# Kernel tuning notes

Hardware: AMD Instinct MI355X
Metric: run time of the kernel (lower is better)

Reference implementation:

```python
import jax, jax.numpy as jnp
import numpy as np

N = 100000   # nodes
E = 1600000  # edges
DIN = 100    # input feature dim
D = 64       # hidden dim per GCN layer
G = 512      # graphs in batch
EPS = 1e-5


def setup_inputs() -> dict:
    key = jax.random.key(0)
    ks = jax.random.split(key, 16)
    inp = {}
    inp["x"] = jax.random.normal(ks[0], (N, DIN), dtype=jnp.float32)
    inp["edge_index"] = jax.random.randint(ks[1], (2, E), 0, N)
    inp["edge_weight"] = jax.random.uniform(ks[2], (E,), dtype=jnp.float32)
    inp["batch"] = jnp.sort(jax.random.randint(ks[3], (N,), 0, G))
    dims = [DIN, D, D, D]
    for i in range(3):
        fan_in = dims[i]
        inp[f"w{i}"] = jax.random.normal(ks[4 + i], (dims[i], dims[i + 1]), dtype=jnp.float32) / np.sqrt(fan_in)
        inp[f"b{i}"] = jnp.zeros((dims[i + 1],), dtype=jnp.float32)
        inp[f"g{i}"] = jnp.ones((dims[i + 1],), dtype=jnp.float32)   # BN scale
        inp[f"be{i}"] = jnp.zeros((dims[i + 1],), dtype=jnp.float32)  # BN shift
    inp["out_w"] = jax.random.normal(ks[7], (D, 1), dtype=jnp.float32) / np.sqrt(D)
    inp["out_b"] = jnp.zeros((1,), dtype=jnp.float32)
    return inp


def reference(x, edge_index, edge_weight, batch,
              w0, b0, g0, be0, w1, b1, g1, be1, w2, b2, g2, be2,
              out_w, out_b):
    src, dst = edge_index[0], edge_index[1]
    n = x.shape[0]
    # GCN symmetric normalization with self-loops (PyG gcn_norm, fill_value=1)
    deg = jnp.zeros((n,), dtype=x.dtype).at[dst].add(edge_weight) + 1.0
    dinv = jax.lax.rsqrt(deg)
    norm = edge_weight * dinv[src] * dinv[dst]   # [E]
    self_coeff = dinv * dinv                      # 1/deg, self-loop norm  [N]

    def gcn_bn_relu(h, w, b, g, be):
        h = h @ w + b                                             # linear transform [N,D]
        msg = norm[:, None] * h[src]                              # gather + weight [E,D]
        agg = jnp.zeros_like(h).at[dst].add(msg) + h * self_coeff[:, None]
        mean = agg.mean(axis=0)
        var = agg.var(axis=0)                                     # biased var (torch BN)
        hn = (agg - mean) * jax.lax.rsqrt(var + EPS) * g + be
        return jax.nn.relu(hn)                                    # dropout p=0 -> identity

    h = gcn_bn_relu(x, w0, b0, g0, be0)
    h = gcn_bn_relu(h, w1, b1, g1, be1)
    h = gcn_bn_relu(h, w2, b2, g2, be2)

    # global mean pool per graph
    sums = jax.ops.segment_sum(h, batch, num_segments=G)
    counts = jax.ops.segment_sum(jnp.ones((n, 1), dtype=h.dtype), batch, num_segments=G)
    pooled = sums / jnp.maximum(counts, 1.0)
    return pooled @ out_w + out_b
```

## Files before the change

kernel.cpp:

```cpp
#include <hip/hip_runtime.h>
#include <hip/hip_fp16.h>
#include <cstdint>

#define DH 64
#define EPSV 1e-5f
#define GBLK 2048
#define NBUK 256
#define BROWS 512
#define BINJ 8
#define CAP 12288

__global__ void k_fill(float* __restrict__ p, float v, size_t n) {
  size_t i = blockIdx.x * (size_t)blockDim.x + threadIdx.x;
  if (i < n) p[i] = v;
}

__global__ void k_gcur0(unsigned* __restrict__ gcur0) {
  gcur0[threadIdx.x] = (unsigned)(threadIdx.x * CAP);
}

__global__ __launch_bounds__(256) void k_bin0(
    const int* __restrict__ src, const int* __restrict__ dst,
    const float* __restrict__ ew, unsigned* __restrict__ gcur0,
    unsigned long long* __restrict__ bstage, int E_) {
  __shared__ unsigned cntL[NBUK], offL[NBUK], runL[NBUK];
  const int t = threadIdx.x;
  const int base = blockIdx.x * (256 * BINJ);
  cntL[t] = 0;
  runL[t] = 0;
  __syncthreads();
  unsigned hi[BINJ], lo[BINJ];
  int bb[BINJ];
#pragma unroll
  for (int j = 0; j < BINJ; ++j) {
    int e = base + j * 256 + t;
    bb[j] = -1;
    if (e < E_) {
      int q = dst[e];
      hi[j] = ((unsigned)(q & (BROWS - 1)) << 17) | (unsigned)src[e];
      lo[j] = __float_as_uint(ew[e]);
      bb[j] = q >> 9;
      atomicAdd(&cntL[bb[j]], 1u);
    }
  }
  __syncthreads();
  offL[t] = cntL[t] ? atomicAdd(&gcur0[t], cntL[t]) : 0u;
  __syncthreads();
#pragma unroll
  for (int j = 0; j < BINJ; ++j) {
    if (bb[j] >= 0) {
      unsigned p = offL[bb[j]] + atomicAdd(&runL[bb[j]], 1u);
      bstage[p] = ((unsigned long long)hi[j] << 32) | lo[j];
    }
  }
}

__global__ __launch_bounds__(256) void k_bcnt(
    const unsigned long long* __restrict__ bstage, const unsigned* __restrict__ gcur0,
    int* __restrict__ cnt, float* __restrict__ dinv, float* __restrict__ sc, int N_) {
  __shared__ unsigned cntL[BROWS], degL[BROWS];
  const int b = blockIdx.x, t = threadIdx.x;
  for (int i = t; i < BROWS; i += 256) {
    cntL[i] = 0;
    degL[i] = 0;
  }
  __syncthreads();
  const unsigned beg = (unsigned)(b * CAP), end = gcur0[b];
  for (unsigned p = beg + t; p < end; p += 256) {
    unsigned long long v = bstage[p];
    unsigned r = (unsigned)(v >> 49);
    float w = __uint_as_float((unsigned)v);
    atomicAdd(&cntL[r], 1u);
    atomicAdd(&degL[r], (unsigned)(w * 16777216.0f));
  }
  __syncthreads();
  for (int i = t; i < BROWS; i += 256) {
    int r = b * BROWS + i;
    if (r < N_) {
      float deg = 1.0f + (float)degL[i] * (1.0f / 16777216.0f);
      cnt[r] = (int)cntL[i];
      dinv[r] = rsqrtf(deg);
      sc[r] = 1.0f / deg;
    }
  }
}

__global__ __launch_bounds__(256) void k_scan1(const int* __restrict__ cnt,
                                               int* __restrict__ out,
                                               int* __restrict__ bsums,
                                               int N_, int n1) {
  __shared__ int sm[256];
  const int t = threadIdx.x;
  const int base = blockIdx.x * 1024 + t * 4;
  int v[4], lsum = 0;
#pragma unroll
  for (int j = 0; j < 4; ++j) {
    int i = base + j;
    v[j] = (i < N_) ? ((cnt[i] + 7) & ~7) : 0;
    lsum += v[j];
  }
  sm[t] = lsum;
  __syncthreads();
  for (int o = 1; o < 256; o <<= 1) {
    int x = (t >= o) ? sm[t - o] : 0;
    __syncthreads();
    if (t >= o) sm[t] += x;
    __syncthreads();
  }
  int run = sm[t] - lsum;
#pragma unroll
  for (int j = 0; j < 4; ++j) {
    int i = base + j;
    if (i < n1) out[i] = run;
    run += v[j];
  }
  if (t == 255) bsums[blockIdx.x] = sm[255];
}

__global__ __launch_bounds__(256) void k_scan2(int* __restrict__ bsums, int nb) {
  __shared__ int sm[256];
  int t = threadIdx.x;
  int v = (t < nb) ? bsums[t] : 0;
  sm[t] = v;
  __syncthreads();
  for (int o = 1; o < 256; o <<= 1) {
    int x = (t >= o) ? sm[t - o] : 0;
    __syncthreads();
    if (t >= o) sm[t] += x;
    __syncthreads();
  }
  if (t < nb) bsums[t] = sm[t] - v;
}

__global__ void k_scan3(int* __restrict__ out, const int* __restrict__ bsums, int n1) {
  int i = blockIdx.x * blockDim.x + threadIdx.x;
  if (i < n1) out[i] += bsums[i >> 10];
}

__global__ __launch_bounds__(256) void k_fin(
    const unsigned long long* __restrict__ bstage, const int* __restrict__ rowstart,
    const unsigned* __restrict__ gcur0, const float* __restrict__ dinv,
    unsigned* __restrict__ elist, int N_) {
  __shared__ unsigned lcur[BROWS];
  __shared__ int rsL[BROWS + 1];
  __shared__ float dvL[BROWS];
  const int b = blockIdx.x, t = threadIdx.x;
  const int r0 = b * BROWS;
  for (int i = t; i < BROWS; i += 256) {
    lcur[i] = 0;
    int r = r0 + i;
    dvL[i] = (r < N_) ? dinv[r] : 0.f;
  }
  for (int i = t; i <= BROWS; i += 256) {
    int r = r0 + i;
    if (r > N_) r = N_;
    rsL[i] = rowstart[r];
  }
  __syncthreads();
  const unsigned beg = (unsigned)(b * CAP), end = gcur0[b];
  for (unsigned p = beg + t; p < end; p += 256) {
    unsigned long long v = bstage[p];
    unsigned hi = (unsigned)(v >> 32);
    unsigned r = hi >> 17;
    unsigned s = hi & 0x1FFFFu;
    float w = __uint_as_float((unsigned)v);
    float nm = w * dinv[s] * dvL[r];
    unsigned h15 = (unsigned)__half_as_ushort(__float2half(nm));
    unsigned slot = (unsigned)rsL[r] + atomicAdd(&lcur[r], 1u);
    elist[slot] = (h15 << 17) | s;
  }
  __syncthreads();
  for (int i = t; i < BROWS; i += 256) {
    unsigned p = (unsigned)rsL[i] + lcur[i];
    const unsigned pe = (unsigned)rsL[i + 1];
    for (; p < pe; ++p) elist[p] = 0u;
  }
}

__global__ void k_gbound(const int* __restrict__ batch, int* __restrict__ gstart,
                         int N_, int G_) {
  int i = blockIdx.x * blockDim.x + threadIdx.x;
  if (i >= N_) return;
  int b = batch[i];
  if (i == 0) {
    for (int g = 0; g <= b; ++g) gstart[g] = 0;
  }
  int nb = (i + 1 < N_) ? batch[i + 1] : G_;
  for (int g = b + 1; g <= nb; ++g) gstart[g] = i + 1;
}

template <typename AT>
__global__ __launch_bounds__(256) void k_gemm(
    const AT* __restrict__ A, const float* __restrict__ W,
    const float* __restrict__ bias, const float* __restrict__ stats,
    const float* __restrict__ gam, const float* __restrict__ bet,
    __half* __restrict__ Hh, int n, int K, int fuse, float invN) {
  __shared__ float As[128][17];
  __shared__ float Bs[16][64];
  __shared__ float saL[DH], sbL[DH];
  const int tid = threadIdx.x;
  const int tx = tid & 7;
  const int ty = tid >> 3;
  const int r0 = blockIdx.x * 128;
  if (fuse && tid < DH) {
    float mean = stats[tid] * invN;
    float var = stats[DH + tid] * invN - mean * mean;
    float a = rsqrtf(var + EPSV) * gam[tid];
    saL[tid] = a;
    sbL[tid] = bet[tid] - mean * a;
  }
  if (fuse) __syncthreads();
  float acc[4][8] = {};
  for (int kc = 0; kc < K; kc += 16) {
    for (int idx = tid; idx < 128 * 16; idx += 256) {
      int r = idx >> 4, c = idx & 15;
      int gr = r0 + r, gc = kc + c;
      float v = (gr < n && gc < K) ? (float)A[(size_t)gr * K + gc] : 0.0f;
      if (fuse) v = fmaxf(v * saL[gc] + sbL[gc], 0.0f);
      As[r][c] = v;
    }
    for (int idx = tid; idx < 16 * 64; idx += 256) {
      int r = idx >> 6, c = idx & 63;
      int gr = kc + r;
      Bs[r][c] = (gr < K) ? W[gr * DH + c] : 0.0f;
    }
    __syncthreads();
#pragma unroll
    for (int kk = 0; kk < 16; ++kk) {
      float a[4], b[8];
#pragma unroll
      for (int i = 0; i < 4; ++i) a[i] = As[ty * 4 + i][kk];
#pragma unroll
      for (int j = 0; j < 8; ++j) b[j] = Bs[kk][tx * 8 + j];
#pragma unroll
      for (int i = 0; i < 4; ++i)
#pragma unroll
        for (int j = 0; j < 8; ++j) acc[i][j] += a[i] * b[j];
    }
    __syncthreads();
  }
#pragma unroll
  for (int i = 0; i < 4; ++i) {
    int gr = r0 + ty * 4 + i;
    if (gr < n) {
      float h[8];
#pragma unroll
      for (int j = 0; j < 8; ++j) h[j] = acc[i][j] + bias[tx * 8 + j];
      uint4 o;
      o.x = (unsigned)__half_as_ushort(__float2half(h[0])) |
            ((unsigned)__half_as_ushort(__float2half(h[1])) << 16);
      o.y = (unsigned)__half_as_ushort(__float2half(h[2])) |
            ((unsigned)__half_as_ushort(__float2half(h[3])) << 16);
      o.z = (unsigned)__half_as_ushort(__float2half(h[4])) |
            ((unsigned)__half_as_ushort(__float2half(h[5])) << 16);
      o.w = (unsigned)__half_as_ushort(__float2half(h[6])) |
            ((unsigned)__half_as_ushort(__float2half(h[7])) << 16);
      *reinterpret_cast<uint4*>(&Hh[(size_t)gr * DH + tx * 8]) = o;
    }
  }
}

__global__ __launch_bounds__(256) void k_gather(
    const unsigned* __restrict__ elist, const int* __restrict__ rowstart,
    const __half* __restrict__ Hh, const float* __restrict__ sc,
    __half* __restrict__ AGGh, float* __restrict__ statp, int n) {
  const int wid = threadIdx.x >> 6;
  const int d = threadIdx.x & 63;
  const int gw = blockIdx.x * 4 + wid;
  const int nw = gridDim.x * 4;
  unsigned short* AGGu = (unsigned short*)AGGh;
  float s = 0.f, ss = 0.f;
  for (int row = gw; row < n; row += nw) {
    const int rs = rowstart[row], re = rowstart[row + 1];
    float acc = __half2float(Hh[(size_t)row * DH + d]) * sc[row];
    for (int base = rs; base < re; base += 64) {
      const int rem = re - base;
      unsigned eL = 0u;
      if (d < rem) eL = __builtin_nontemporal_load(&elist[base + d]);
      const int m = rem < 64 ? rem : 64;
      for (int j = 0; j < m; j += 8) {
#pragma unroll
        for (int jj = 0; jj < 8; ++jj) {
          const unsigned e = __shfl(eL, j + jj, 64);
          const float v = __half2float(Hh[(size_t)(e & 0x1FFFFu) * DH + d]);
          const float nm =
              __half2float(__ushort_as_half((unsigned short)(e >> 17)));
          acc = fmaf(nm, v, acc);
        }
      }
    }
    __builtin_nontemporal_store(__half_as_ushort(__float2half(acc)),
                                &AGGu[(size_t)row * DH + d]);
    s += acc;
    ss += acc * acc;
  }
  __shared__ float sm[4][DH], sm2[4][DH];
  sm[wid][d] = s;
  sm2[wid][d] = ss;
  __syncthreads();
  if (threadIdx.x < DH) {
    float a = sm[0][d] + sm[1][d] + sm[2][d] + sm[3][d];
    float b = sm2[0][d] + sm2[1][d] + sm2[2][d] + sm2[3][d];
    __builtin_nontemporal_store(a, &statp[(size_t)blockIdx.x * 128 + d]);
    __builtin_nontemporal_store(b, &statp[(size_t)blockIdx.x * 128 + DH + d]);
  }
}

__global__ __launch_bounds__(256) void k_redstats(const float* __restrict__ statp,
                                                  float* __restrict__ stats, int nblk) {
  const int t = blockIdx.x;
  float s = 0.f;
  for (int b = threadIdx.x; b < nblk; b += 256) s += statp[(size_t)b * 128 + t];
#pragma unroll
  for (int o = 32; o > 0; o >>= 1) s += __shfl_down(s, o, 64);
  __shared__ float sm[4];
  if ((threadIdx.x & 63) == 0) sm[threadIdx.x >> 6] = s;
  __syncthreads();
  if (threadIdx.x == 0) stats[t] = sm[0] + sm[1] + sm[2] + sm[3];
}

__global__ __launch_bounds__(256) void k_poolhead(
    const __half* __restrict__ AGGh, const float* __restrict__ stats,
    const float* __restrict__ gam, const float* __restrict__ bet,
    const float* __restrict__ ow, const int* __restrict__ gstart,
    const float* __restrict__ ob, float* __restrict__ out, float invN) {
  const int g = blockIdx.x;
  const int gs = gstart[g], ge = gstart[g + 1];
  const int wid = threadIdx.x >> 6;
  const int d = threadIdx.x & 63;
  float mean = stats[d] * invN;
  float var = stats[DH + d] * invN - mean * mean;
  float sa = rsqrtf(var + EPSV) * gam[d];
  float sb = bet[d] - mean * sa;
  const float w = ow[d];
  float acc = 0.f;
  for (int row = gs + wid; row < ge; row += 4)
    acc += fmaxf(__half2float(AGGh[(size_t)row * DH + d]) * sa + sb, 0.f) * w;
#pragma unroll
  for (int off = 32; off > 0; off >>= 1) acc += __shfl_down(acc, off, 64);
  __shared__ float sm[4];
  if (d == 0) sm[wid] = acc;
  __syncthreads();
  if (threadIdx.x == 0) {
    float s = sm[0] + sm[1] + sm[2] + sm[3];
    float cnt = (float)(ge - gs);
    out[g] = s / fmaxf(cnt, 1.0f) + ob[0];
  }
}

extern "C" void kernel_launch(void* const* d_in, const int* in_sizes, int n_in,
                              void* d_out, int out_size, void* d_ws, size_t ws_size,
                              hipStream_t stream) {
  const float* x    = (const float*)d_in[0];
  const int*   ei   = (const int*)d_in[1];
  const float* ew   = (const float*)d_in[2];
  const int*   batch= (const int*)d_in[3];
  const float* w0   = (const float*)d_in[4];
  const float* b0   = (const float*)d_in[5];
  const float* g0   = (const float*)d_in[6];
  const float* be0  = (const float*)d_in[7];
  const float* w1   = (const float*)d_in[8];
  const float* b1   = (const float*)d_in[9];
  const float* g1   = (const float*)d_in[10];
  const float* be1  = (const float*)d_in[11];
  const float* w2   = (const float*)d_in[12];
  const float* b2   = (const float*)d_in[13];
  const float* g2   = (const float*)d_in[14];
  const float* be2  = (const float*)d_in[15];
  const float* ow   = (const float*)d_in[16];
  const float* ob   = (const float*)d_in[17];

  const int N_  = in_sizes[3];
  const int E_  = in_sizes[2];
  const int DIN_= in_sizes[0] / N_;
  const int G_  = out_size;
  const int* srcIdx = ei;
  const int* dstIdx = ei + E_;
  const int n1 = N_ + 1;
  const size_t epad = (size_t)E_ + 7ull * N_;

  float* ws = (float*)d_ws;
  size_t off = 0;
  unsigned long long* bstage = (unsigned long long*)(ws + off);
  off += (size_t)2 * NBUK * CAP;
  unsigned* elist = (unsigned*)(ws + off); off += epad;
  float* dinv     = ws + off; off += N_;
  float* sc       = ws + off; off += N_;
  int*   cnt      = (int*)(ws + off); off += N_;
  int*   rowstart = (int*)(ws + off); off += n1 + 1;
  int*   bsums    = (int*)(ws + off); off += 256;
  unsigned* gcur0 = (unsigned*)(ws + off); off += NBUK;
  int*   gstart   = (int*)(ws + off); off += G_ + 1;
  __half* hhalf   = (__half*)(ws + off); off += (size_t)N_ * DH / 2;
  __half* aggh    = (__half*)(ws + off); off += (size_t)N_ * DH / 2;
  float* stats    = ws + off; off += 2 * DH;
  float* statp    = ws + off; off += (size_t)GBLK * 128;
  (void)ws_size; (void)n_in;

  k_gcur0<<<1, NBUK, 0, stream>>>(gcur0);
  k_bin0<<<(E_ + 256 * BINJ - 1) / (256 * BINJ), 256, 0, stream>>>(
      srcIdx, dstIdx, ew, gcur0, bstage, E_);
  k_bcnt<<<NBUK, 256, 0, stream>>>(bstage, gcur0, cnt, dinv, sc, N_);

  const int nb = (n1 + 1023) / 1024;
  k_scan1<<<nb, 256, 0, stream>>>(cnt, rowstart, bsums, N_, n1);
  k_scan2<<<1, 256, 0, stream>>>(bsums, nb);
  k_scan3<<<(n1 + 255) / 256, 256, 0, stream>>>(rowstart, bsums, n1);

  k_fin<<<NBUK, 256, 0, stream>>>(bstage, rowstart, gcur0, dinv, elist, N_);

  k_gbound<<<(N_ + 255) / 256, 256, 0, stream>>>(batch, gstart, N_, G_);

  const float* Wl[3]  = {w0, w1, w2};
  const float* Bl[3]  = {b0, b1, b2};
  const float* Gl[3]  = {g0, g1, g2};
  const float* BeL[3] = {be0, be1, be2};

  const float invN = 1.0f / (float)N_;

  for (int l = 0; l < 3; ++l) {
    if (l == 0) {
      k_gemm<float><<<(N_ + 127) / 128, 256, 0, stream>>>(
          x, Wl[0], Bl[0], stats, nullptr, nullptr, hhalf, N_, DIN_, 0, invN);
    } else {
      k_gemm<__half><<<(N_ + 127) / 128, 256, 0, stream>>>(
          aggh, Wl[l], Bl[l], stats, Gl[l - 1], BeL[l - 1], hhalf, N_, DH, 1, invN);
    }
    k_gather<<<GBLK, 256, 0, stream>>>(elist, rowstart, hhalf, sc, aggh, statp, N_);
    k_redstats<<<128, 256, 0, stream>>>(statp, stats, GBLK);
  }

  k_poolhead<<<G_, 256, 0, stream>>>(aggh, stats, g2, be2, ow, gstart, ob,
                                     (float*)d_out, invN);
}
```

Measured before the change: 385.0 us.

## Replace FP32 SIMT dense transform GEMM with FP16 MFMA kernel

Rewrites the per-layer linear transform to use 16x16x32 f16 MFMA instructions. A and W tiles are staged in LDS as fp16 with an XOR swizzle, K is padded to 128 or 64, and the fused BN+ReLU prologue is kept. The goal is to cut the ALU cost of the dense GEMMs. In exchange it rounds the layer-0 input x and the weights to fp16, and the output is written as scattered 2-byte stores instead of 16-byte vector stores.

```diff
diff --git a/kernel.cpp b/kernel.cpp
--- a/kernel.cpp
+++ b/kernel.cpp
@@ -9,6 +9,9 @@
 #define BROWS 512
 #define BINJ 8
 #define CAP 12288
+
+typedef _Float16 half8 __attribute__((ext_vector_type(8)));
+typedef float f32x4 __attribute__((ext_vector_type(4)));
 
 __global__ void k_fill(float* __restrict__ p, float v, size_t n) {
   size_t i = blockIdx.x * (size_t)blockDim.x + threadIdx.x;
@@ -189,73 +192,103 @@
   for (int g = b + 1; g <= nb; ++g) gstart[g] = i + 1;
 }
 
-template <typename AT>
-__global__ __launch_bounds__(256) void k_gemm(
-    const AT* __restrict__ A, const float* __restrict__ W,
+template <int KP, int FUSE>
+__global__ __launch_bounds__(256) void k_gemm_mfma(
+    const void* __restrict__ Ap, const float* __restrict__ W,
     const float* __restrict__ bias, const float* __restrict__ stats,
     const float* __restrict__ gam, const float* __restrict__ bet,
-    __half* __restrict__ Hh, int n, int K, int fuse, float invN) {
-  __shared__ float As[128][17];
-  __shared__ float Bs[16][64];
+    __half* __restrict__ Hh, int n, int Kreal, float invN) {
+  __shared__ _Float16 Ah[128 * KP];
+  __shared__ _Float16 Bt[64 * KP];
   __shared__ float saL[DH], sbL[DH];
   const int tid = threadIdx.x;
-  const int tx = tid & 7;
-  const int ty = tid >> 3;
   const int r0 = blockIdx.x * 128;
-  if (fuse && tid < DH) {
-    float mean = stats[tid] * invN;
-    float var = stats[DH + tid] * invN - mean * mean;
-    float a = rsqrtf(var + EPSV) * gam[tid];
-    saL[tid] = a;
-    sbL[tid] = bet[tid] - mean * a;
-  }
-  if (fuse) __syncthreads();
-  float acc[4][8] = {};
-  for (int kc = 0; kc < K; kc += 16) {
-    for (int idx = tid; idx < 128 * 16; idx += 256) {
-      int r = idx >> 4, c = idx & 15;
-      int gr = r0 + r, gc = kc + c;
-      float v = (gr < n && gc < K) ? (float)A[(size_t)gr * K + gc] : 0.0f;
-      if (fuse) v = fmaxf(v * saL[gc] + sbL[gc], 0.0f);
-      As[r][c] = v;
-    }
-    for (int idx = tid; idx < 16 * 64; idx += 256) {
-      int r = idx >> 6, c = idx & 63;
-      int gr = kc + r;
-      Bs[r][c] = (gr < K) ? W[gr * DH + c] : 0.0f;
+  if (FUSE) {
+    if (tid < DH) {
+      float mean = stats[tid] * invN;
+      float var = stats[DH + tid] * invN - mean * mean;
+      float a = rsqrtf(var + EPSV) * gam[tid];
+      saL[tid] = a;
+      sbL[tid] = bet[tid] - mean * a;
     }
     __syncthreads();
-#pragma unroll
-    for (int kk = 0; kk < 16; ++kk) {
-      float a[4], b[8];
-#pragma unroll
-      for (int i = 0; i < 4; ++i) a[i] = As[ty * 4 + i][kk];
-#pragma unroll
-      for (int j = 0; j < 8; ++j) b[j] = Bs[kk][tx * 8 + j];
-#pragma unroll
-      for (int i = 0; i < 4; ++i)
-#pragma unroll
-        for (int j = 0; j < 8; ++j) acc[i][j] += a[i] * b[j];
-    }
-    __syncthreads();
-  }
-#pragma unroll
-  for (int i = 0; i < 4; ++i) {
-    int gr = r0 + ty * 4 + i;
-    if (gr < n) {
-      float h[8];
-#pragma unroll
-      for (int j = 0; j < 8; ++j) h[j] = acc[i][j] + bias[tx * 8 + j];
-      uint4 o;
-      o.x = (unsigned)__half_as_ushort(__float2half(h[0])) |
-            ((unsigned)__half_as_ushort(__float2half(h[1])) << 16);
-      o.y = (unsigned)__half_as_ushort(__float2half(h[2])) |
-            ((unsigned)__half_as_ushort(__float2half(h[3])) << 16);
-      o.z = (unsigned)__half_as_ushort(__float2half(h[4])) |
-            ((unsigned)__half_as_ushort(__float2half(h[5])) << 16);
-      o.w = (unsigned)__half_as_ushort(__float2half(h[6])) |
-            ((unsigned)__half_as_ushort(__float2half(h[7])) << 16);
-      *reinterpret_cast<uint4*>(&Hh[(size_t)gr * DH + tx * 8]) = o;
+  }
+  constexpr int KC = KP / 8;
+  for (int ci = tid; ci < 128 * KC; ci += 256) {
+    int row = ci / KC, kc = ci % KC;
+    int gr = r0 + row, k0 = kc * 8;
+    half8 hv;
+    if (FUSE) {
+      const unsigned short* Aa = (const unsigned short*)Ap;
+#pragma unroll
+      for (int j = 0; j < 8; ++j) {
+        int k = k0 + j;
+        float a = (gr < n) ? __half2float(__ushort_as_half(Aa[(size_t)gr * DH + k])) : 0.f;
+        hv[j] = (_Float16)fmaxf(a * saL[k] + sbL[k], 0.f);
+      }
+    } else {
+      const float* Ax = (const float*)Ap;
+#pragma unroll
+      for (int j = 0; j < 8; ++j) {
+        int k = k0 + j;
+        float a = (gr < n && k < Kreal) ? Ax[(size_t)gr * Kreal + k] : 0.f;
+        hv[j] = (_Float16)a;
+      }
+    }
+    *(half8*)&Ah[row * KP + (k0 ^ ((row & 7) * 8))] = hv;
+  }
+  for (int ci = tid; ci < 64 * KC; ci += 256) {
+    int c = ci / KC, kc = ci % KC, k0 = kc * 8;
+    half8 wv;
+#pragma unroll
+    for (int j = 0; j < 8; ++j) {
+      int k = k0 + j;
+      wv[j] = (_Float16)((k < Kreal) ? W[k * DH + c] : 0.f);
+    }
+    *(half8*)&Bt[c * KP + (k0 ^ ((c & 7) * 8))] = wv;
+  }
+  __syncthreads();
+  const int w = tid >> 6, l = tid & 63;
+  const int lr = l & 15, lg = l >> 4;
+  f32x4 acc[2][4];
+#pragma unroll
+  for (int a1 = 0; a1 < 2; ++a1)
+#pragma unroll
+    for (int a2 = 0; a2 < 4; ++a2) acc[a1][a2] = (f32x4){0.f, 0.f, 0.f, 0.f};
+#pragma unroll
+  for (int ks = 0; ks < KP / 32; ++ks) {
+    const int k0 = ks * 32 + lg * 8;
+    half8 av[2], bv[4];
+#pragma unroll
+    for (int rf = 0; rf < 2; ++rf) {
+      int row = w * 32 + rf * 16 + lr;
+      av[rf] = *(const half8*)&Ah[row * KP + (k0 ^ ((row & 7) * 8))];
+    }
+#pragma unroll
+    for (int cf = 0; cf < 4; ++cf) {
+      int col = cf * 16 + lr;
+      bv[cf] = *(const half8*)&Bt[col * KP + (k0 ^ ((col & 7) * 8))];
+    }
+#pragma unroll
+    for (int rf = 0; rf < 2; ++rf)
+#pragma unroll
+      for (int cf = 0; cf < 4; ++cf)
+        acc[rf][cf] =
+            __builtin_amdgcn_mfma_f32_16x16x32_f16(av[rf], bv[cf], acc[rf][cf], 0, 0, 0);
+  }
+  unsigned short* Hu = (unsigned short*)Hh;
+#pragma unroll
+  for (int rf = 0; rf < 2; ++rf) {
+#pragma unroll
+    for (int cf = 0; cf < 4; ++cf) {
+      int col = cf * 16 + lr;
+      float bcol = bias[col];
+#pragma unroll
+      for (int i = 0; i < 4; ++i) {
+        int row = r0 + w * 32 + rf * 16 + lg * 4 + i;
+        if (row < n)
+          Hu[(size_t)row * DH + col] = __half_as_ushort(__float2half(acc[rf][cf][i] + bcol));
+      }
     }
   }
 }
@@ -417,14 +450,15 @@
   const float* BeL[3] = {be0, be1, be2};
 
   const float invN = 1.0f / (float)N_;
+  const int gblk = (N_ + 127) / 128;
 
   for (int l = 0; l < 3; ++l) {
     if (l == 0) {
-      k_gemm<float><<<(N_ + 127) / 128, 256, 0, stream>>>(
-          x, Wl[0], Bl[0], stats, nullptr, nullptr, hhalf, N_, DIN_, 0, invN);
+      k_gemm_mfma<128, 0><<<gblk, 256, 0, stream>>>(
+          (const void*)x, Wl[0], Bl[0], stats, nullptr, nullptr, hhalf, N_, DIN_, invN);
     } else {
-      k_gemm<__half><<<(N_ + 127) / 128, 256, 0, stream>>>(
-          aggh, Wl[l], Bl[l], stats, Gl[l - 1], BeL[l - 1], hhalf, N_, DH, 1, invN);
+      k_gemm_mfma<64, 1><<<gblk, 256, 0, stream>>>(
+          (const void*)aggh, Wl[l], Bl[l], stats, Gl[l - 1], BeL[l - 1], hhalf, N_, DH, invN);
     }
     k_gather<<<GBLK, 256, 0, stream>>>(elist, rowstart, hhalf, sc, aggh, statp, N_);
     k_redstats<<<128, 256, 0, stream>>>(statp, stats, GBLK);
```

Measured after the change: 373.6 us. 3.0% less time.
